# Kernel optimization log

Measured on AMD Instinct MI355X. Metric: run time of the kernel, lower is better.

The kernel has to match this reference:

```python
import jax, jax.numpy as jnp
import numpy as np

N_NODES = 4096  # nodes per graph (output1 reshaped to [-1, N_NODES])


def setup_inputs() -> dict:
    key = jax.random.key(0)
    ks = jax.random.split(key, 10)
    total_nodes = 64 * N_NODES          # 64 graphs of 4096 nodes
    n_edges = total_nodes * 8           # avg degree 8 lattice-like graph
    n_hidden = 128
    return {
        "node_features": jax.random.normal(ks[0], (total_nodes, 1), jnp.float32),
        "src": jax.random.randint(ks[1], (n_edges,), 0, total_nodes, jnp.int32),
        "dst": jax.random.randint(ks[2], (n_edges,), 0, total_nodes, jnp.int32),
        "w_self1": jax.random.normal(ks[3], (1, n_hidden), jnp.float32) * 0.5,
        "w_neigh1": jax.random.normal(ks[4], (1, n_hidden), jnp.float32) * 0.5,
        "b1": jnp.zeros((n_hidden,), jnp.float32),
        "w_self2": jax.random.normal(ks[5], (n_hidden, 1), jnp.float32) * (1.0 / np.sqrt(n_hidden)),
        "w_neigh2": jax.random.normal(ks[6], (n_hidden, 1), jnp.float32) * (1.0 / np.sqrt(n_hidden)),
        "b2": jnp.zeros((1,), jnp.float32),
        "w3": jax.random.normal(ks[7], (N_NODES, N_NODES), jnp.float32) * (1.0 / np.sqrt(N_NODES)),
        "b3": jnp.zeros((N_NODES,), jnp.float32),
    }


def _sage_mean(feat, src, dst, w_self, w_neigh, b, num_nodes):
    # gather source-node features along edges, mean-reduce at destination
    agg = jax.ops.segment_sum(feat[src], dst, num_segments=num_nodes)
    deg = jax.ops.segment_sum(jnp.ones((src.shape[0], 1), feat.dtype), dst,
                              num_segments=num_nodes)
    h_neigh = agg / jnp.maximum(deg, 1.0)
    return feat @ w_self + h_neigh @ w_neigh + b


def reference(node_features, src, dst, w_self1, w_neigh1, b1,
              w_self2, w_neigh2, b2, w3, b3):
    n = node_features.shape[0]
    h1 = jnp.tanh(_sage_mean(node_features, src, dst, w_self1, w_neigh1, b1, n))
    out1 = _sage_mean(h1, src, dst, w_self2, w_neigh2, b2, n)
    output1 = out1.reshape(-1, N_NODES)          # [batch, n_nodes]
    h2 = jnp.tanh(output1)
    output2 = h2 @ w3 + b3
    return (output1, output2)
```

## Files before the change

### kernel.cpp

```cpp
#include <hip/hip_runtime.h>


#define NTOT (64 * 4096)
#define NHID 128
#define GK   4096
#define KCH  256
#define KCHUNKS 16
#define NBINS 1024
#define BSZ   256
#define BSH   8
#define CAP   2432
#define SCB   256
#define GB    10

typedef unsigned int u32;

__device__ __forceinline__ float fast_tanh(float x) {
    float ax = fabsf(x);
    float t  = __expf(-2.0f * ax);
    float r  = (1.0f - t) * __builtin_amdgcn_rcpf(1.0f + t);
    return copysignf(r, x);
}


__global__ void __launch_bounds__(1024) scatter_x(const int* __restrict__ src,
                                                  const int* __restrict__ dst,
                                                  int n_edges,
                                                  int* __restrict__ edge_cnt,
                                                  u32* __restrict__ packed) {
    __shared__ int lc[NBINS];
    __shared__ int lbase[NBINS];
    int t = threadIdx.x;
    lc[t] = 0;
    __syncthreads();
    int per = (n_edges + gridDim.x - 1) / gridDim.x;
    int e0 = blockIdx.x * per;
    int e1 = min(e0 + per, n_edges);

    int dreg[8], sreg[8];
#pragma unroll
    for (int i = 0; i < 8; ++i) {
        int e = e0 + t + i * 1024;
        bool ok = e < e1;
        int d = ok ? dst[e] : -1;
        dreg[i] = d;
        sreg[i] = ok ? src[e] : 0;
        if (ok) atomicAdd(&lc[d >> BSH], 1);
    }
    __syncthreads();
    lbase[t] = atomicAdd(&edge_cnt[t], lc[t]);
    lc[t] = 0;
    __syncthreads();
#pragma unroll
    for (int i = 0; i < 8; ++i) {
        int d = dreg[i];
        if (d >= 0) {
            int b = d >> BSH;
            int pos = lbase[b] + atomicAdd(&lc[b], 1);
            if (pos < CAP)
                packed[(size_t)b * CAP + pos] =
                    ((u32)(d & (BSZ - 1)) << 18) | (u32)sreg[i];
        }
    }
}

__global__ void __launch_bounds__(256) agn1_x(const u32* __restrict__ packed,
                                              const int* __restrict__ edge_cnt,
                                              const float* __restrict__ nf,
                                              const float* __restrict__ w_s1,
                                              const float* __restrict__ w_n1,
                                              const float* __restrict__ bb1,
                                              const float* __restrict__ w_s2,
                                              const float* __restrict__ w_n2,
                                              float* __restrict__ degf,
                                              float* __restrict__ selfp,
                                              float* __restrict__ sp) {
    __shared__ float lsum[BSZ];
    __shared__ float lcnt[BSZ];
    __shared__ float lws1[NHID], lwn1[NHID], lb1[NHID], lws2[NHID], lwn2[NHID];
    int t = threadIdx.x;
    int b = blockIdx.x;
    lsum[t] = 0.0f;
    lcnt[t] = 0.0f;
    if (t < NHID) {
        lws1[t] = w_s1[t];
        lwn1[t] = w_n1[t];
        lb1[t]  = bb1[t];
        lws2[t] = w_s2[t];
        lwn2[t] = w_n2[t];
    }
    __syncthreads();
    int en = min(edge_cnt[b], CAP);
    const u32* pk = packed + (size_t)b * CAP;

    u32  pr[GB];
    float gv[GB];
#pragma unroll
    for (int i = 0; i < GB; ++i) {
        int e = t + i * BSZ;
        pr[i] = (e < en) ? pk[e] : 0xFFFFFFFFu;
    }
#pragma unroll
    for (int i = 0; i < GB; ++i)
        gv[i] = (pr[i] != 0xFFFFFFFFu) ? nf[pr[i] & 0x3FFFFu] : 0.0f;
#pragma unroll
    for (int i = 0; i < GB; ++i) {
        if (pr[i] != 0xFFFFFFFFu) {
            int local = (int)(pr[i] >> 18);
            atomicAdd(&lsum[local], gv[i]);
            atomicAdd(&lcnt[local], 1.0f);
        }
    }
    __syncthreads();

    int v = b * BSZ + t;
    float cf = lcnt[t];
    float hn = lsum[t] / fmaxf(cf, 1.0f);
    float f  = nf[v];
    float a = 0.0f, s2 = 0.0f;
#pragma unroll 8
    for (int j = 0; j < NHID; ++j) {
        float th = fast_tanh(fmaf(f, lws1[j], fmaf(hn, lwn1[j], lb1[j])));
        a  = fmaf(th, lws2[j], a);
        s2 = fmaf(th, lwn2[j], s2);
    }
    degf[v]  = cf;
    selfp[v] = a;
    sp[v]    = s2;
}

__global__ void __launch_bounds__(256) agn2_x(const u32* __restrict__ packed,
                                              const int* __restrict__ edge_cnt,
                                              const float* __restrict__ spv,
                                              const float* __restrict__ selfp,
                                              const float* __restrict__ degf,
                                              const float* __restrict__ b2p,
                                              float* __restrict__ out1,
                                              float* __restrict__ h2t) {
    __shared__ float lsum[BSZ];
    int t = threadIdx.x;
    int b = blockIdx.x;
    lsum[t] = 0.0f;
    __syncthreads();
    int en = min(edge_cnt[b], CAP);
    const u32* pk = packed + (size_t)b * CAP;

    u32  pr[GB];
    float gv[GB];
#pragma unroll
    for (int i = 0; i < GB; ++i) {
        int e = t + i * BSZ;
        pr[i] = (e < en) ? pk[e] : 0xFFFFFFFFu;
    }
#pragma unroll
    for (int i = 0; i < GB; ++i)
        gv[i] = (pr[i] != 0xFFFFFFFFu) ? spv[pr[i] & 0x3FFFFu] : 0.0f;
#pragma unroll
    for (int i = 0; i < GB; ++i) {
        if (pr[i] != 0xFFFFFFFFu)
            atomicAdd(&lsum[pr[i] >> 18], gv[i]);
    }
    __syncthreads();

    int v = b * BSZ + t;
    float o = selfp[v] + lsum[t] / fmaxf(degf[v], 1.0f) + b2p[0];
    out1[v] = o;
    int r = v >> 12;
    int k = v & 4095;
    h2t[k * 64 + r] = fast_tanh(o);
}

__global__ void __launch_bounds__(512, 4) gemm_x(const float* __restrict__ h2t,
                                                 const float* __restrict__ w3,
                                                 float* __restrict__ Cpart) {
    int lane = threadIdx.x & 63;
    int wv   = threadIdx.x >> 6;
    int col  = blockIdx.x * 64 + lane;
    int k0   = blockIdx.y * KCH;
    int row0 = __builtin_amdgcn_readfirstlane(wv * 8);

    const float* Ap = h2t + (size_t)k0 * 64 + row0;
    const float* wp = w3 + (size_t)k0 * GK + col;

    float acc[8];
#pragma unroll
    for (int r = 0; r < 8; ++r) acc[r] = 0.0f;

    float bvA[8], bvB[8];
    float avA[8], avB[8];

#pragma unroll
    for (int j = 0; j < 8; ++j) bvA[j] = wp[(size_t)j * GK];
#pragma unroll
    for (int r = 0; r < 8; ++r) avA[r] = Ap[r];

    for (int kk = 0; kk < KCH; kk += 16) {
#pragma unroll
        for (int j = 0; j < 8; ++j) bvB[j] = wp[(size_t)(kk + 8 + j) * GK];
#pragma unroll
        for (int j = 0; j < 8; ++j) {
            const float* An = Ap + (size_t)(kk + j + 1) * 64;
            if ((j & 1) == 0) {
#pragma unroll
                for (int r = 0; r < 8; ++r) avB[r] = An[r];
                float b = bvA[j];
#pragma unroll
                for (int r = 0; r < 8; ++r) acc[r] = fmaf(avA[r], b, acc[r]);
            } else {
#pragma unroll
                for (int r = 0; r < 8; ++r) avA[r] = An[r];
                float b = bvA[j];
#pragma unroll
                for (int r = 0; r < 8; ++r) acc[r] = fmaf(avB[r], b, acc[r]);
            }
        }
        if (kk + 16 < KCH) {
#pragma unroll
            for (int j = 0; j < 8; ++j) bvA[j] = wp[(size_t)(kk + 16 + j) * GK];
        }
#pragma unroll
        for (int j = 0; j < 8; ++j) {
            int kn = kk + 8 + j + 1;
            if (kn > KCH - 1) kn = KCH - 1;
            const float* An = Ap + (size_t)kn * 64;
            if ((j & 1) == 0) {
#pragma unroll
                for (int r = 0; r < 8; ++r) avB[r] = An[r];
                float b = bvB[j];
#pragma unroll
                for (int r = 0; r < 8; ++r) acc[r] = fmaf(avA[r], b, acc[r]);
            } else {
#pragma unroll
                for (int r = 0; r < 8; ++r) avA[r] = An[r];
                float b = bvB[j];
#pragma unroll
                for (int r = 0; r < 8; ++r) acc[r] = fmaf(avB[r], b, acc[r]);
            }
        }
    }

    float* Cp = Cpart + (size_t)blockIdx.y * NTOT + (size_t)row0 * GK + col;
#pragma unroll
    for (int r = 0; r < 8; ++r) Cp[(size_t)r * GK] = acc[r];
}

__global__ void reduce_x(const float4* __restrict__ Cpart, const float4* __restrict__ b3v,
                         float4* __restrict__ out2) {
    int v = blockIdx.x * blockDim.x + threadIdx.x;
    float4 s = b3v[v & 1023];
#pragma unroll
    for (int kc = 0; kc < KCHUNKS; ++kc) {
        float4 c = Cpart[(size_t)kc * (NTOT / 4) + v];
        s.x += c.x; s.y += c.y; s.z += c.z; s.w += c.w;
    }
    out2[v] = s;
}


__global__ void edge_pass1_f(const int* __restrict__ src, const int* __restrict__ dst,
                             const float* __restrict__ nf, float* __restrict__ agg,
                             float* __restrict__ deg, int n_edges) {
    int e = blockIdx.x * blockDim.x + threadIdx.x;
    if (e >= n_edges) return;
    int s = src[e], d = dst[e];
    atomicAdd(&agg[d], nf[s]);
    atomicAdd(&deg[d], 1.0f);
}

__global__ void node1_f(const float* __restrict__ nf, float* s0,
                        const float* __restrict__ deg,
                        const float* __restrict__ w_s1, const float* __restrict__ w_n1,
                        const float* __restrict__ bb1,
                        const float* __restrict__ w_s2, const float* __restrict__ w_n2,
                        float* __restrict__ sp) {
    __shared__ float lws1[NHID], lwn1[NHID], lb1[NHID], lws2[NHID], lwn2[NHID];
    int tid = threadIdx.x;
    if (tid < NHID) {
        lws1[tid] = w_s1[tid];
        lwn1[tid] = w_n1[tid];
        lb1[tid]  = bb1[tid];
        lws2[tid] = w_s2[tid];
        lwn2[tid] = w_n2[tid];
    }
    __syncthreads();
    int v = blockIdx.x * blockDim.x + tid;
    float f  = nf[v];
    float hn = s0[v] / fmaxf(deg[v], 1.0f);
    float a = 0.0f, s = 0.0f;
#pragma unroll 8
    for (int j = 0; j < NHID; ++j) {
        float t = fast_tanh(fmaf(f, lws1[j], fmaf(hn, lwn1[j], lb1[j])));
        a = fmaf(t, lws2[j], a);
        s = fmaf(t, lwn2[j], s);
    }
    s0[v] = a;
    sp[v] = s;
}

__global__ void edge_pass2_f(const int* __restrict__ src, const int* __restrict__ dst,
                             const float* __restrict__ sp, float* __restrict__ agg2,
                             int n_edges) {
    int e = blockIdx.x * blockDim.x + threadIdx.x;
    if (e >= n_edges) return;
    atomicAdd(&agg2[dst[e]], sp[src[e]]);
}

__global__ void node2_f(const float* __restrict__ s0, const float* __restrict__ agg2,
                        const float* __restrict__ deg, const float* __restrict__ b2p,
                        const float* __restrict__ b3p,
                        float* __restrict__ out1, float* __restrict__ h2t,
                        float* __restrict__ out2) {
    int v = blockIdx.x * blockDim.x + threadIdx.x;
    float o = s0[v] + agg2[v] / fmaxf(deg[v], 1.0f) + b2p[0];
    out1[v] = o;
    int r = v >> 12;
    int k = v & 4095;
    h2t[k * 64 + r] = fast_tanh(o);
    out2[v] = b3p[v & 4095];
}

__global__ void __launch_bounds__(256) gemm_f(const float* __restrict__ h2t,
                                              const float* __restrict__ w3,
                                              float* __restrict__ out2) {
    int n  = blockIdx.x * 256 + threadIdx.x;
    int k0 = blockIdx.y * KCH;
    float acc[64];
#pragma unroll
    for (int r = 0; r < 64; ++r) acc[r] = 0.0f;
    for (int k = k0; k < k0 + KCH; ++k) {
        float bv = w3[(size_t)k * GK + n];
        const float* Ak = h2t + k * 64;
#pragma unroll
        for (int r = 0; r < 64; ++r) acc[r] = fmaf(Ak[r], bv, acc[r]);
    }
#pragma unroll
    for (int r = 0; r < 64; ++r) atomicAdd(&out2[r * GK + n], acc[r]);
}


extern "C" void kernel_launch(void* const* d_in, const int* in_sizes, int n_in,
                              void* d_out, int out_size, void* d_ws, size_t ws_size,
                              hipStream_t stream) {
    const float* nf  = (const float*)d_in[0];
    const int*   src = (const int*)d_in[1];
    const int*   dst = (const int*)d_in[2];
    const float* ws1 = (const float*)d_in[3];
    const float* wn1 = (const float*)d_in[4];
    const float* b1  = (const float*)d_in[5];
    const float* ws2 = (const float*)d_in[6];
    const float* wn2 = (const float*)d_in[7];
    const float* b2  = (const float*)d_in[8];
    const float* w3  = (const float*)d_in[9];
    const float* b3  = (const float*)d_in[10];
    float* out1 = (float*)d_out;
    float* out2 = (float*)d_out + NTOT;

    int n_edges = in_sizes[1];
    int eb = (n_edges + 255) / 256;

    if (ws_size >= (size_t)20 * 1024 * 1024 && n_edges <= (1 << 21)) {
        char*  base     = (char*)d_ws;
        u32*   packed   = (u32*)base;
        float* degf     = (float*)(base + 10485760);
        float* selfp    = (float*)(base + 11534336);
        float* spbuf    = (float*)(base + 12582912);
        float* h2t      = (float*)(base + 16777216);
        int*   edge_cnt = (int*)(base + 17825792);
        float* Cpart    = (float*)base;

        (void)hipMemsetAsync(edge_cnt, 0, NBINS * sizeof(int), stream);
        scatter_x<<<SCB, 1024, 0, stream>>>(src, dst, n_edges, edge_cnt, packed);
        agn1_x<<<NBINS, BSZ, 0, stream>>>(packed, edge_cnt, nf, ws1, wn1, b1,
                                          ws2, wn2, degf, selfp, spbuf);
        agn2_x<<<NBINS, BSZ, 0, stream>>>(packed, edge_cnt, spbuf, selfp, degf,
                                          b2, out1, h2t);
        gemm_x<<<dim3(GK / 64, KCHUNKS), 512, 0, stream>>>(h2t, w3, Cpart);
        reduce_x<<<NTOT / 4 / 256, 256, 0, stream>>>((const float4*)Cpart,
                                                     (const float4*)b3, (float4*)out2);
    } else {
        float* ws = (float*)d_ws;
        float* S0 = ws;
        float* S1 = ws + 1 * NTOT;
        float* S2 = ws + 2 * NTOT;
        float* S3 = ws + 3 * NTOT;

        (void)hipMemsetAsync(S0, 0, (size_t)3 * NTOT * sizeof(float), stream);
        edge_pass1_f<<<eb, 256, 0, stream>>>(src, dst, nf, S0, S1, n_edges);
        node1_f<<<NTOT / 256, 256, 0, stream>>>(nf, S0, S1, ws1, wn1, b1, ws2, wn2, S3);
        edge_pass2_f<<<eb, 256, 0, stream>>>(src, dst, S3, S2, n_edges);
        node2_f<<<NTOT / 256, 256, 0, stream>>>(S0, S2, S1, b2, b3, out1, S3, out2);
        gemm_f<<<dim3(GK / 256, KCHUNKS), 256, 0, stream>>>(S3, w3, out2);
    }
}
```

Measured before the change: 232.0 us.

## Process two bins per agn1 block to overlap gathers with tanh compute

Each agn1 block now handles two destination bins, issuing the second bin's packed-edge and feature gathers before running the first bin's 128-wide tanh MLP, so global latency hides behind compute. The grid is halved to compensate. Separately, the scatter kernel rotates which bin each thread atomically reserves by block index, spreading global atomic contention on edge_cnt. In exchange, each block holds more registers and there are fewer blocks to fill the GPU.

```diff
diff --git a/kernel.cpp b/kernel.cpp
--- a/kernel.cpp
+++ b/kernel.cpp
@@ -48,8 +48,9 @@
         if (ok) atomicAdd(&lc[d >> BSH], 1);
     }
     __syncthreads();
-    lbase[t] = atomicAdd(&edge_cnt[t], lc[t]);
-    lc[t] = 0;
+    int myb = (t + blockIdx.x * 17) & (NBINS - 1);
+    lbase[myb] = atomicAdd(&edge_cnt[myb], lc[myb]);
+    lc[myb] = 0;
     __syncthreads();
 #pragma unroll
     for (int i = 0; i < 8; ++i) {
@@ -75,13 +76,14 @@
                                               float* __restrict__ degf,
                                               float* __restrict__ selfp,
                                               float* __restrict__ sp) {
-    __shared__ float lsum[BSZ];
-    __shared__ float lcnt[BSZ];
+    __shared__ float lsum[2][BSZ];
+    __shared__ float lcnt[2][BSZ];
     __shared__ float lws1[NHID], lwn1[NHID], lb1[NHID], lws2[NHID], lwn2[NHID];
-    int t = threadIdx.x;
-    int b = blockIdx.x;
-    lsum[t] = 0.0f;
-    lcnt[t] = 0.0f;
+    int t  = threadIdx.x;
+    int b0 = blockIdx.x * 2;
+    int b1 = b0 + 1;
+    lsum[0][t] = 0.0f; lcnt[0][t] = 0.0f;
+    lsum[1][t] = 0.0f; lcnt[1][t] = 0.0f;
     if (t < NHID) {
         lws1[t] = w_s1[t];
         lwn1[t] = w_n1[t];
@@ -89,44 +91,92 @@
         lws2[t] = w_s2[t];
         lwn2[t] = w_n2[t];
     }
-    __syncthreads();
-    int en = min(edge_cnt[b], CAP);
-    const u32* pk = packed + (size_t)b * CAP;
-
-    u32  pr[GB];
-    float gv[GB];
+    int enA = min(edge_cnt[b0], CAP);
+    int enB = min(edge_cnt[b1], CAP);
+    const u32* pkA = packed + (size_t)b0 * CAP;
+    const u32* pkB = packed + (size_t)b1 * CAP;
+
+    u32  prA[GB];
+    float gvA[GB];
 #pragma unroll
     for (int i = 0; i < GB; ++i) {
         int e = t + i * BSZ;
-        pr[i] = (e < en) ? pk[e] : 0xFFFFFFFFu;
+        prA[i] = (e < enA) ? pkA[e] : 0xFFFFFFFFu;
     }
 #pragma unroll
     for (int i = 0; i < GB; ++i)
-        gv[i] = (pr[i] != 0xFFFFFFFFu) ? nf[pr[i] & 0x3FFFFu] : 0.0f;
-#pragma unroll
-    for (int i = 0; i < GB; ++i) {
-        if (pr[i] != 0xFFFFFFFFu) {
-            int local = (int)(pr[i] >> 18);
-            atomicAdd(&lsum[local], gv[i]);
-            atomicAdd(&lcnt[local], 1.0f);
-        }
-    }
-    __syncthreads();
-
-    int v = b * BSZ + t;
-    float cf = lcnt[t];
-    float hn = lsum[t] / fmaxf(cf, 1.0f);
-    float f  = nf[v];
-    float a = 0.0f, s2 = 0.0f;
+        gvA[i] = (prA[i] != 0xFFFFFFFFu) ? nf[prA[i] & 0x3FFFFu] : 0.0f;
+
+    __syncthreads();
+
+#pragma unroll
+    for (int i = 0; i < GB; ++i) {
+        if (prA[i] != 0xFFFFFFFFu) {
+            int l = (int)(prA[i] >> 18);
+            atomicAdd(&lsum[0][l], gvA[i]);
+            atomicAdd(&lcnt[0][l], 1.0f);
+        }
+    }
+
+    u32  prB[GB];
+    float gvB[GB];
+#pragma unroll
+    for (int i = 0; i < GB; ++i) {
+        int e = t + i * BSZ;
+        prB[i] = (e < enB) ? pkB[e] : 0xFFFFFFFFu;
+    }
+#pragma unroll
+    for (int i = 0; i < GB; ++i)
+        gvB[i] = (prB[i] != 0xFFFFFFFFu) ? nf[prB[i] & 0x3FFFFu] : 0.0f;
+
+    asm volatile("s_waitcnt lgkmcnt(0)" ::: "memory");
+    __builtin_amdgcn_s_barrier();
+
+    {
+        int v = b0 * BSZ + t;
+        float cf = lcnt[0][t];
+        float hn = lsum[0][t] / fmaxf(cf, 1.0f);
+        float f  = nf[v];
+        float a = 0.0f, s2 = 0.0f;
 #pragma unroll 8
-    for (int j = 0; j < NHID; ++j) {
-        float th = fast_tanh(fmaf(f, lws1[j], fmaf(hn, lwn1[j], lb1[j])));
-        a  = fmaf(th, lws2[j], a);
-        s2 = fmaf(th, lwn2[j], s2);
-    }
-    degf[v]  = cf;
-    selfp[v] = a;
-    sp[v]    = s2;
+        for (int j = 0; j < NHID; ++j) {
+            float th = fast_tanh(fmaf(f, lws1[j], fmaf(hn, lwn1[j], lb1[j])));
+            a  = fmaf(th, lws2[j], a);
+            s2 = fmaf(th, lwn2[j], s2);
+        }
+        degf[v]  = cf;
+        selfp[v] = a;
+        sp[v]    = s2;
+    }
+
+#pragma unroll
+    for (int i = 0; i < GB; ++i) {
+        if (prB[i] != 0xFFFFFFFFu) {
+            int l = (int)(prB[i] >> 18);
+            atomicAdd(&lsum[1][l], gvB[i]);
+            atomicAdd(&lcnt[1][l], 1.0f);
+        }
+    }
+
+    asm volatile("s_waitcnt lgkmcnt(0)" ::: "memory");
+    __builtin_amdgcn_s_barrier();
+
+    {
+        int v = b1 * BSZ + t;
+        float cf = lcnt[1][t];
+        float hn = lsum[1][t] / fmaxf(cf, 1.0f);
+        float f  = nf[v];
+        float a = 0.0f, s2 = 0.0f;
+#pragma unroll 8
+        for (int j = 0; j < NHID; ++j) {
+            float th = fast_tanh(fmaf(f, lws1[j], fmaf(hn, lwn1[j], lb1[j])));
+            a  = fmaf(th, lws2[j], a);
+            s2 = fmaf(th, lwn2[j], s2);
+        }
+        degf[v]  = cf;
+        selfp[v] = a;
+        sp[v]    = s2;
+    }
 }
 
 __global__ void __launch_bounds__(256) agn2_x(const u32* __restrict__ packed,
@@ -370,8 +420,8 @@
 
         (void)hipMemsetAsync(edge_cnt, 0, NBINS * sizeof(int), stream);
         scatter_x<<<SCB, 1024, 0, stream>>>(src, dst, n_edges, edge_cnt, packed);
-        agn1_x<<<NBINS, BSZ, 0, stream>>>(packed, edge_cnt, nf, ws1, wn1, b1,
-                                          ws2, wn2, degf, selfp, spbuf);
+        agn1_x<<<NBINS / 2, BSZ, 0, stream>>>(packed, edge_cnt, nf, ws1, wn1, b1,
+                                              ws2, wn2, degf, selfp, spbuf);
         agn2_x<<<NBINS, BSZ, 0, stream>>>(packed, edge_cnt, spbuf, selfp, degf,
                                           b2, out1, h2t);
         gemm_x<<<dim3(GK / 64, KCHUNKS), 512, 0, stream>>>(h2t, w3, Cpart);
```

Result: no change. 233.8 us (+0.8%).
